# Kernel optimization log

Hardware: AMD Instinct MI355X
Metric: run time of the kernel (lower is better)

## Reference

```python
import jax, jax.numpy as jnp
import numpy as np

HEAD_SIZE = 256
ROTARY_DIM = 64
ROPE_THETA = 10000.0


def apply_gptj_rope(x, positions):
    """GPT-J (interleaved, non-neox) rotary embedding.
    x: [B, S, H, D], positions: [B, S] int. Rotates first ROTARY_DIM dims."""
    half = ROTARY_DIM // 2
    inv_freq = 1.0 / (ROPE_THETA ** (jnp.arange(0, ROTARY_DIM, 2, dtype=jnp.float32) / ROTARY_DIM))
    ang = positions.astype(jnp.float32)[..., None] * inv_freq      # [B, S, half]
    cos = jnp.cos(ang)[:, :, None, :]                               # [B, S, 1, half]
    sin = jnp.sin(ang)[:, :, None, :]
    xr, xp = x[..., :ROTARY_DIM], x[..., ROTARY_DIM:]
    x1, x2 = xr[..., 0::2], xr[..., 1::2]                           # interleaved pairs
    o1 = x1 * cos - x2 * sin
    o2 = x2 * cos + x1 * sin
    rot = jnp.stack([o1, o2], axis=-1).reshape(*xr.shape)           # re-interleave
    return jnp.concatenate([rot, xp], axis=-1)


def setup_inputs() -> dict:
    key = jax.random.key(0)
    k1, k2, k3 = jax.random.split(key, 3)
    B, S, H = 2, 2048, 4096
    position_ids = jnp.broadcast_to(jnp.arange(S, dtype=jnp.int32), (B, S))
    hidden_states = jax.random.normal(k1, (B, S, H), dtype=jnp.float32)
    Wqkv = jax.random.normal(k2, (H, 3 * H), dtype=jnp.float32) * (H ** -0.5)
    Wo = jax.random.normal(k3, (H, H), dtype=jnp.float32) * (H ** -0.5)
    return {"position_ids": position_ids, "hidden_states": hidden_states, "Wqkv": Wqkv, "Wo": Wo}


def reference(position_ids, hidden_states, Wqkv, Wo):
    B, S, H = hidden_states.shape
    nh = H // HEAD_SIZE
    qkv = hidden_states @ Wqkv                                      # [B, S, 3H]
    q, k, v = jnp.split(qkv, 3, axis=-1)
    q = apply_gptj_rope(q.reshape(B, S, nh, HEAD_SIZE), position_ids)
    k = apply_gptj_rope(k.reshape(B, S, nh, HEAD_SIZE), position_ids)
    v = v.reshape(B, S, nh, HEAD_SIZE)
    scale = HEAD_SIZE ** -0.5
    scores = jnp.einsum('bqhd,bkhd->bhqk', q, k) * scale            # [B, nh, S, S]
    causal = jnp.tril(jnp.ones((S, S), dtype=bool))
    scores = jnp.where(causal, scores, jnp.finfo(scores.dtype).min)
    attn = jax.nn.softmax(scores, axis=-1)
    ctx = jnp.einsum('bhqk,bkhd->bqhd', attn, v).reshape(B, S, H)
    return ctx @ Wo
```

## Files before the change

### kernel.cpp

```cpp
#include <hip/hip_runtime.h>
#include <hip/hip_bf16.h>

typedef __bf16 bf16x8 __attribute__((ext_vector_type(8)));
typedef float f32x4 __attribute__((ext_vector_type(4)));

#define MFMA_BF16(a,b,c) __builtin_amdgcn_mfma_f32_16x16x32_bf16(a,b,c,0,0,0)

#define GLOAD16(g, l) __builtin_amdgcn_global_load_lds( \
    (const __attribute__((address_space(1))) unsigned int*)(g), \
    (__attribute__((address_space(3))) unsigned int*)(l), 16, 0, 0)

__device__ __forceinline__ unsigned short f2bf(float f) {
  unsigned u = __builtin_bit_cast(unsigned, f);
  return (unsigned short)((u + 0x7FFFu + ((u >> 16) & 1u)) >> 16);
}

__global__ __launch_bounds__(256)
void convert_bf16(const float* __restrict__ src, unsigned short* __restrict__ dst,
                  int n8) {
  int i = blockIdx.x * blockDim.x + threadIdx.x;
  int stride = gridDim.x * blockDim.x;
  for (; i < n8; i += stride) {
    float4 a = ((const float4*)src)[i*2];
    float4 b = ((const float4*)src)[i*2 + 1];
    short4 h0, h1;
    h0.x = (short)f2bf(a.x); h0.y = (short)f2bf(a.y);
    h0.z = (short)f2bf(a.z); h0.w = (short)f2bf(a.w);
    h1.x = (short)f2bf(b.x); h1.y = (short)f2bf(b.y);
    h1.z = (short)f2bf(b.z); h1.w = (short)f2bf(b.w);
    ((short4*)dst)[i*2] = h0;
    ((short4*)dst)[i*2 + 1] = h1;
  }
}

__global__ __launch_bounds__(256)
void transpose_convert(const float* __restrict__ W, unsigned short* __restrict__ Wt,
                       int K, int N) {
  __shared__ float tl[64][65];
  const int k0 = blockIdx.y * 64, n0 = blockIdx.x * 64;
  const int tr = threadIdx.x >> 4;
  const int tc4 = (threadIdx.x & 15) * 4;
  for (int i = 0; i < 4; ++i) {
    int r = tr + i*16;
    float4 v = *(const float4*)(W + (size_t)(k0 + r)*N + n0 + tc4);
    tl[r][tc4+0] = v.x; tl[r][tc4+1] = v.y;
    tl[r][tc4+2] = v.z; tl[r][tc4+3] = v.w;
  }
  __syncthreads();
  for (int i = 0; i < 4; ++i) {
    int nr = tr + i*16;
    short4 h;
    h.x = (short)f2bf(tl[tc4+0][nr]);
    h.y = (short)f2bf(tl[tc4+1][nr]);
    h.z = (short)f2bf(tl[tc4+2][nr]);
    h.w = (short)f2bf(tl[tc4+3][nr]);
    *(short4*)(Wt + (size_t)(n0 + nr)*K + k0 + tc4) = h;
  }
}

__global__ __launch_bounds__(256)
void transpose_v(const unsigned short* __restrict__ qkv,
                 unsigned short* __restrict__ Vt) {
  __shared__ unsigned short tl[64][68];
  const int bh = blockIdx.z;
  const int s0 = blockIdx.x * 64;
  const int d0 = blockIdx.y * 64;
  const int b = bh >> 4, h = bh & 15;
  const int tr = threadIdx.x >> 4;
  const int tc = (threadIdx.x & 15) * 4;
  const unsigned short* src = qkv + ((size_t)(b*2048 + s0))*12288 + 8192 + h*256 + d0;
  for (int i = 0; i < 4; ++i) {
    int s = tr + i*16;
    *(short4*)&tl[s][tc] = *(const short4*)(src + (size_t)s*12288 + tc);
  }
  __syncthreads();
  unsigned short* dst = Vt + ((size_t)bh*256 + d0)*2048 + s0;
  for (int i = 0; i < 4; ++i) {
    int d = tr + i*16;
    short4 h4;
    h4.x = (short)tl[tc+0][d];
    h4.y = (short)tl[tc+1][d];
    h4.z = (short)tl[tc+2][d];
    h4.w = (short)tl[tc+3][d];
    *(short4*)(dst + (size_t)d*2048 + tc) = h4;
  }
}

template<bool ROPE, bool OUT_BF16>
__global__ __launch_bounds__(512, 2)
void gemm256(const unsigned short* __restrict__ A,
             const unsigned short* __restrict__ Bt,
             const int* __restrict__ pos,
             void* __restrict__ Cp, int N, int K, int nbx)
{
  __shared__ __align__(16) unsigned short L[2][4][8192];
  const int tid = threadIdx.x, lane = tid & 63, w = tid >> 6;
  const int wr = w >> 2, wc = w & 3;
  const int nwg = gridDim.x;
  int wg = blockIdx.x;
  if ((nwg & 7) == 0) wg = (wg & 7) * (nwg >> 3) + (wg >> 3);
  const int bx = wg % nbx, by = wg / nbx;
  const int row0 = by * 256, col0 = bx * 256;

  const int crow = lane & 15, g = lane >> 4;
  const int arow = lane >> 3;
  const int asegsw = ((lane & 7) ^ arow) * 8;
  const int xo = (crow & 7) << 4;

  unsigned aoff[4], boff[4];
#pragma unroll
  for (int i = 0; i < 4; ++i) {
    int chunk = w*4 + i;
    aoff[i] = (unsigned)((row0 + chunk*8 + arow) * K + asegsw);
    boff[i] = (unsigned)((col0 + chunk*8 + arow) * K + asegsw);
  }

#define STAGE(T, B) do {                                              \
    int kto = (T) * 64;                                               \
    _Pragma("unroll")                                                 \
    for (int i = 0; i < 4; ++i) {                                     \
      GLOAD16(A  + aoff[i] + kto, &L[B][wr][(wc*4 + i)*512]);         \
      GLOAD16(Bt + boff[i] + kto, &L[B][2 + wr][(wc*4 + i)*512]);     \
    }                                                                 \
  } while (0)

  f32x4 acc[8][4] = {};
  const int nt = K >> 6;
  STAGE(0, 0);
  STAGE(1, 1);
  int cur = 0;

  for (int t = 0; t < nt; ++t) {
    if (t < nt - 1) asm volatile("s_waitcnt vmcnt(8)" ::: "memory");
    else            asm volatile("s_waitcnt vmcnt(0)" ::: "memory");
    __builtin_amdgcn_s_barrier();

    const char* Ab = (const char*)&L[cur][wr][0];
    const char* Bb = (const char*)&L[cur][2 + (wc >> 1)][0];
    const int rB0 = (wc & 1) * 64;

    __builtin_amdgcn_s_setprio(1);
    bf16x8 af[2][8], bfv[2][4];
#pragma unroll
    for (int kk = 0; kk < 2; ++kk) {
      const int ko = (((kk*4 + g) << 4)) ^ xo;
#pragma unroll
      for (int m = 0; m < 8; ++m)
        af[kk][m] = *(const bf16x8*)(Ab + (m*16 + crow)*128 + ko);
#pragma unroll
      for (int n = 0; n < 4; ++n)
        bfv[kk][n] = *(const bf16x8*)(Bb + (rB0 + n*16 + crow)*128 + ko);
    }
#pragma unroll
    for (int kk = 0; kk < 2; ++kk)
#pragma unroll
      for (int m = 0; m < 8; ++m)
#pragma unroll
        for (int n = 0; n < 4; ++n)
          acc[m][n] = MFMA_BF16(af[kk][m], bfv[kk][n], acc[m][n]);
    __builtin_amdgcn_s_setprio(0);

    __builtin_amdgcn_sched_barrier(0);
    asm volatile("s_waitcnt lgkmcnt(0)" ::: "memory");
    __builtin_amdgcn_sched_barrier(0);
    __builtin_amdgcn_s_barrier();
    if (t + 2 < nt) STAGE(t + 2, cur);
    cur ^= 1;
  }
#undef STAGE

#pragma unroll
  for (int m = 0; m < 8; ++m) {
    const int rbase = row0 + wr*128 + m*16 + (g << 2);
#pragma unroll
    for (int n = 0; n < 4; ++n) {
      const int c = col0 + wc*64 + n*16 + crow;
      bool rot = false;
      float invf = 0.f;
      if (ROPE) {
        rot = (c < 8192) && ((c & 255) < 64);
        if (rot) {
          int i2 = (c & 63) >> 1;
          invf = exp2f(-(float)i2 * 0.4152410118609203f);
        }
      }
#pragma unroll
      for (int r = 0; r < 4; ++r) {
        int rowg = rbase + r;
        float v = acc[m][n][r];
        if (ROPE && rot) {
          float ang = (float)pos[rowg] * invf;
          float s_ = __sinf(ang), c_ = __cosf(ang);
          float pv = __shfl_xor(v, 1, 64);
          v = (c & 1) ? fmaf(v, c_, pv * s_) : fmaf(v, c_, -pv * s_);
        }
        if (OUT_BF16)
          ((unsigned short*)Cp)[(size_t)rowg*N + c] = f2bf(v);
        else
          ((float*)Cp)[(size_t)rowg*N + c] = v;
      }
    }
  }
}

template<bool A_BF16, bool ROPE, bool OUT_BF16>
__global__ __launch_bounds__(256)
void gemm128(const void* __restrict__ Ap, const float* __restrict__ Bp,
             const int* __restrict__ pos, void* __restrict__ Cp,
             int N, int K)
{
  __shared__ __align__(16) short Al[128*40];
  __shared__ __align__(16) short Bl[128*40];
  const int tid = threadIdx.x;
  const int lane = tid & 63, wid = tid >> 6;
  const int wr = wid >> 1, wc = wid & 1;
  const int row0 = blockIdx.y * 128, col0 = blockIdx.x * 128;
  f32x4 acc[4][4] = {};
  const int bcol = tid & 127;
  const int kb0 = (tid >> 7) * 4;

  for (int kt = 0; kt < K; kt += 32) {
    if (A_BF16) {
      const unsigned short* Ab = (const unsigned short*)Ap;
      for (int i = 0; i < 2; ++i) {
        int idx = tid + i*256;
        int ar = idx >> 2, ac = (idx & 3) * 8;
        *(int4*)(&Al[ar*40 + ac]) = *(const int4*)(Ab + (size_t)(row0+ar)*K + kt + ac);
      }
    } else {
      const float* Af = (const float*)Ap;
      for (int i = 0; i < 4; ++i) {
        int idx = tid + i*256;
        int ar = idx >> 3, ac = (idx & 7) * 4;
        float4 v = *(const float4*)(Af + (size_t)(row0+ar)*K + kt + ac);
        short4 h;
        h.x = (short)f2bf(v.x); h.y = (short)f2bf(v.y);
        h.z = (short)f2bf(v.z); h.w = (short)f2bf(v.w);
        *(short4*)(&Al[ar*40 + ac]) = h;
      }
    }
    for (int r = 0; r < 4; ++r) {
      int kb = kb0 + r*8;
      const float* bp = Bp + (size_t)(kt+kb)*N + col0 + bcol;
      float x0 = bp[0];
      float x1 = bp[(size_t)N];
      float x2 = bp[2*(size_t)N];
      float x3 = bp[3*(size_t)N];
      short4 h;
      h.x = (short)f2bf(x0); h.y = (short)f2bf(x1);
      h.z = (short)f2bf(x2); h.w = (short)f2bf(x3);
      *(short4*)(&Bl[bcol*40 + kb]) = h;
    }
    __syncthreads();
    const int k8 = (lane >> 4) * 8;
    bf16x8 af[4], bfr[4];
    for (int m = 0; m < 4; ++m)
      af[m] = *(const bf16x8*)(&Al[(wr*64 + m*16 + (lane&15))*40 + k8]);
    for (int n = 0; n < 4; ++n)
      bfr[n] = *(const bf16x8*)(&Bl[(wc*64 + n*16 + (lane&15))*40 + k8]);
    for (int m = 0; m < 4; ++m)
      for (int n = 0; n < 4; ++n)
        acc[m][n] = MFMA_BF16(af[m], bfr[n], acc[m][n]);
    __syncthreads();
  }

  for (int m = 0; m < 4; ++m) {
    const int rbase = row0 + wr*64 + m*16 + ((lane>>4)<<2);
    for (int n = 0; n < 4; ++n) {
      const int c = col0 + wc*64 + n*16 + (lane & 15);
      bool rot = false;
      float invf = 0.f;
      if (ROPE) {
        rot = (c < 8192) && ((c & 255) < 64);
        if (rot) {
          int i2 = (c & 63) >> 1;
          invf = exp2f(-(float)i2 * 0.4152410118609203f);
        }
      }
      for (int r = 0; r < 4; ++r) {
        int rowg = rbase + r;
        float v = acc[m][n][r];
        if (ROPE && rot) {
          float ang = (float)pos[rowg] * invf;
          float s_ = __sinf(ang), c_ = __cosf(ang);
          float pv = __shfl_xor(v, 1, 64);
          v = (c & 1) ? fmaf(v, c_, pv * s_) : fmaf(v, c_, -pv * s_);
        }
        if (OUT_BF16)
          ((unsigned short*)Cp)[(size_t)rowg*N + c] = f2bf(v);
        else
          ((float*)Cp)[(size_t)rowg*N + c] = v;
      }
    }
  }
}

__global__ __launch_bounds__(512, 2)
void attn_kernel3(const unsigned short* __restrict__ qkv,
                  const unsigned short* __restrict__ Vt,
                  unsigned short* __restrict__ ctx)
{
  const int QN = 12288;
  __shared__ __align__(16) unsigned char Kl[2][32768];
  __shared__ __align__(16) unsigned char Vl[2][32768];
  __shared__ __align__(16) unsigned char Pl[128*144];
  const int tid = threadIdx.x, lane = tid & 63, w = tid >> 6;
  const int qp = blockIdx.x, bh = blockIdx.y;
  const int b = bh >> 4, h = bh & 15;
  const size_t rowbase = (size_t)b * 2048;
  const int colr = lane & 15, g = lane >> 4;

  const int kr0 = tid >> 5;
  const int kcolb = ((tid*16) & 511) ^ ((kr0 & 7) << 4);
  const unsigned koff = (unsigned)(kr0*QN) + (kcolb >> 1);
  const int vd0 = tid >> 3;
  const int vcolb = ((tid*16) & 127) ^ ((vd0 & 7) << 4);
  const unsigned voff = (unsigned)(vd0*2048) + (vcolb >> 1);

  const unsigned short* kbase = qkv + rowbase*QN + 4096 + h*256;
  const unsigned short* vbase = Vt + (size_t)bh*256*2048;

#define STAGEKV(KT, B) do {                                                    \
    const unsigned short* kb_ = kbase + (unsigned)(KT)*64u*(unsigned)QN;       \
    const unsigned short* vb_ = vbase + (unsigned)(KT)*64u;                    \
    _Pragma("unroll")                                                          \
    for (int i = 0; i < 4; ++i)                                                \
      GLOAD16(kb_ + koff + i*16*QN, &Kl[B][tid*16 + i*8192]);                  \
    _Pragma("unroll")                                                          \
    for (int i = 0; i < 4; ++i)                                                \
      GLOAD16(vb_ + voff + i*64*2048, &Vl[B][tid*16 + i*8192]);                \
  } while (0)

  for (int phase = 0; phase < 2; ++phase) {
    const int qt = phase ? qp : (15 - qp);
    const int nkt = 2*qt + 2;

    bf16x8 qf[8];
    {
      const unsigned short* qp_ = qkv + (rowbase + qt*128 + w*16 + colr)*QN + h*256 + g*8;
#pragma unroll
      for (int f = 0; f < 8; ++f)
        qf[f] = *(const bf16x8*)(qp_ + 32*f);
    }
    f32x4 acc[16] = {};
    float m_r[4], l_r[4];
#pragma unroll
    for (int r = 0; r < 4; ++r) { m_r[r] = -1e30f; l_r[r] = 0.f; }

    STAGEKV(0, 0);
    STAGEKV(1, 1);
    int cur = 0;

    for (int kt = 0; kt < nkt; ++kt) {
      if (kt < nkt - 1) asm volatile("s_waitcnt vmcnt(8)" ::: "memory");
      else              asm volatile("s_waitcnt vmcnt(0)" ::: "memory");
      __builtin_amdgcn_s_barrier();

      const unsigned char* Kb = Kl[cur];
      f32x4 sc[4];
      __builtin_amdgcn_s_setprio(1);
#pragma unroll
      for (int nf = 0; nf < 4; ++nf) {
        f32x4 s = {};
        int krow = nf*16 + colr;
        int xo2 = (krow & 7) << 4;
        const unsigned char* kp = Kb + krow*512;
#pragma unroll
        for (int st = 0; st < 8; ++st) {
          bf16x8 kf = *(const bf16x8*)(kp + ((64*st + 16*g) ^ xo2));
          s = MFMA_BF16(qf[st], kf, s);
        }
        sc[nf] = s;
      }
      __builtin_amdgcn_s_setprio(0);

      const int qrow0 = qt*128 + w*16 + g*4;
      float pm[4] = {-3e38f,-3e38f,-3e38f,-3e38f};
      float pvv[4][4];
#pragma unroll
      for (int nf = 0; nf < 4; ++nf) {
        int kcol = kt*64 + nf*16 + colr;
#pragma unroll
        for (int r = 0; r < 4; ++r) {
          float v = sc[nf][r] * 0.0625f;
          if (kcol > qrow0 + r) v = -1e30f;
          pvv[nf][r] = v;
          pm[r] = fmaxf(pm[r], v);
        }
      }
#pragma unroll
      for (int mk = 1; mk < 16; mk <<= 1)
#pragma unroll
        for (int r = 0; r < 4; ++r)
          pm[r] = fmaxf(pm[r], __shfl_xor(pm[r], mk, 64));
      float alpha[4];
#pragma unroll
      for (int r = 0; r < 4; ++r) {
        float mn = fmaxf(m_r[r], pm[r]);
        alpha[r] = __expf(m_r[r] - mn);
        m_r[r] = mn;
      }
      float ps[4] = {0.f,0.f,0.f,0.f};
      unsigned short pb[4][4];
#pragma unroll
      for (int nf = 0; nf < 4; ++nf)
#pragma unroll
        for (int r = 0; r < 4; ++r) {
          float p = __expf(pvv[nf][r] - m_r[r]);
          ps[r] += p;
          pb[nf][r] = f2bf(p);
        }
#pragma unroll
      for (int mk = 1; mk < 16; mk <<= 1)
#pragma unroll
        for (int r = 0; r < 4; ++r)
          ps[r] += __shfl_xor(ps[r], mk, 64);
#pragma unroll
      for (int r = 0; r < 4; ++r)
        l_r[r] = l_r[r]*alpha[r] + ps[r];
#pragma unroll
      for (int nf2 = 0; nf2 < 16; ++nf2)
#pragma unroll
        for (int r = 0; r < 4; ++r)
          acc[nf2][r] *= alpha[r];

#pragma unroll
      for (int nf = 0; nf < 4; ++nf)
#pragma unroll
        for (int r = 0; r < 4; ++r)
          *(unsigned short*)(Pl + (w*16 + g*4 + r)*144 + (nf*16 + colr)*2) = pb[nf][r];

      const unsigned char* Vb = Vl[cur];
      __builtin_amdgcn_s_setprio(1);
#pragma unroll
      for (int st2 = 0; st2 < 2; ++st2) {
        bf16x8 pf = *(const bf16x8*)(Pl + (w*16 + colr)*144 + (32*st2 + g*8)*2);
#pragma unroll
        for (int nf2 = 0; nf2 < 16; ++nf2) {
          int d = nf2*16 + colr;
          bf16x8 vf = *(const bf16x8*)(Vb + ((d*128 + 64*st2 + 16*g) ^ ((d&7)<<4)));
          acc[nf2] = MFMA_BF16(pf, vf, acc[nf2]);
        }
      }
      __builtin_amdgcn_s_setprio(0);

      __builtin_amdgcn_sched_barrier(0);
      asm volatile("s_waitcnt lgkmcnt(0)" ::: "memory");
      __builtin_amdgcn_sched_barrier(0);
      __builtin_amdgcn_s_barrier();
      if (kt + 2 < nkt) STAGEKV(kt + 2, cur);
      cur ^= 1;
    }

    float linv[4];
#pragma unroll
    for (int r = 0; r < 4; ++r) linv[r] = 1.0f / l_r[r];
#pragma unroll
    for (int nf2 = 0; nf2 < 16; ++nf2)
#pragma unroll
      for (int r = 0; r < 4; ++r) {
        int qrow = qt*128 + w*16 + g*4 + r;
        float o = acc[nf2][r] * linv[r];
        ctx[(rowbase + qrow)*4096 + h*256 + nf2*16 + colr] = f2bf(o);
      }
  }
#undef STAGEKV
}

__global__ __launch_bounds__(256, 2)
void attn_kernel2(const unsigned short* __restrict__ qkv,
                  unsigned short* __restrict__ ctx)
{
  const int S = 2048, D = 256, QN = 12288;
  __shared__ __align__(16) unsigned char Kl[64*512];
  __shared__ __align__(16) unsigned char Vl[256*128];
  __shared__ __align__(16) unsigned char Pl[64*144];
  const int tid = threadIdx.x, lane = tid & 63, w = tid >> 6;
  const int qp = blockIdx.x, bh = blockIdx.y;
  const int b = bh >> 4, h = bh & 15;
  const size_t rowbase = (size_t)b * S;
  const int colr = lane & 15, g = lane >> 4;

  const int kr0 = tid >> 5, c8 = (tid & 31) * 8;
  const unsigned kwb = (unsigned)((kr0*512 + c8*2) ^ ((kr0 & 7) << 4));
  const int dd = (tid >> 2) * 4, kbb = (tid & 3) * 4;

  const unsigned short* kbase0 = qkv + rowbase*QN + 4096 + h*D;
  const unsigned short* vbase0 = qkv + rowbase*QN + 8192 + h*D;

  bf16x8 kreg[8];
  short4 vreg[16];

#define LOADKV(KT) do {                                                        \
    const unsigned short* kb_ = kbase0 + (size_t)(KT)*64*QN;                   \
    _Pragma("unroll")                                                          \
    for (int i = 0; i < 8; ++i)                                                \
      kreg[i] = *(const bf16x8*)(kb_ + (size_t)(kr0 + i*8)*QN + c8);           \
    const unsigned short* vb_ = vbase0 + (size_t)(KT)*64*QN;                   \
    _Pragma("unroll")                                                          \
    for (int r4 = 0; r4 < 4; ++r4) {                                           \
      int kb2 = kbb + 16*r4;                                                   \
      _Pragma("unroll")                                                        \
      for (int j = 0; j < 4; ++j)                                              \
        vreg[r4*4+j] = *(const short4*)(vb_ + (size_t)(kb2+j)*QN + dd);        \
    }                                                                          \
  } while (0)

#define WRITEKV() do {                                                         \
    _Pragma("unroll")                                                          \
    for (int i = 0; i < 8; ++i)                                                \
      *(bf16x8*)(Kl + kwb + i*4096) = kreg[i];                                 \
    _Pragma("unroll")                                                          \
    for (int r4 = 0; r4 < 4; ++r4) {                                           \
      int kb2 = kbb + 16*r4;                                                   \
      short4 v0 = vreg[r4*4+0], v1 = vreg[r4*4+1];                             \
      short4 v2 = vreg[r4*4+2], v3 = vreg[r4*4+3];                             \
      short4 t;                                                                \
      t.x=v0.x; t.y=v1.x; t.z=v2.x; t.w=v3.x;                                  \
      *(short4*)(Vl + (((dd+0)*128 + kb2*2) ^ (((dd+0)&7)<<4))) = t;           \
      t.x=v0.y; t.y=v1.y; t.z=v2.y; t.w=v3.y;                                  \
      *(short4*)(Vl + (((dd+1)*128 + kb2*2) ^ (((dd+1)&7)<<4))) = t;           \
      t.x=v0.z; t.y=v1.z; t.z=v2.z; t.w=v3.z;                                  \
      *(short4*)(Vl + (((dd+2)*128 + kb2*2) ^ (((dd+2)&7)<<4))) = t;           \
      t.x=v0.w; t.y=v1.w; t.z=v2.w; t.w=v3.w;                                  \
      *(short4*)(Vl + (((dd+3)*128 + kb2*2) ^ (((dd+3)&7)<<4))) = t;           \
    }                                                                          \
  } while (0)

  for (int phase = 0; phase < 2; ++phase) {
    const int qt = phase ? qp : (31 - qp);

    bf16x8 qf[8];
    {
      const unsigned short* qp_ = qkv + (rowbase + qt*64 + w*16 + colr)*QN + h*D + g*8;
#pragma unroll
      for (int f = 0; f < 8; ++f)
        qf[f] = *(const bf16x8*)(qp_ + 32*f);
    }
    f32x4 acc[16] = {};
    float m_r[4], l_r[4];
#pragma unroll
    for (int r = 0; r < 4; ++r) { m_r[r] = -1e30f; l_r[r] = 0.f; }

    LOADKV(0);
    WRITEKV();
    __syncthreads();

    for (int kt = 0; kt <= qt; ++kt) {
      if (kt < qt) LOADKV(kt + 1);
      __builtin_amdgcn_sched_barrier(0);

      f32x4 sc[4];
#pragma unroll
      for (int nf = 0; nf < 4; ++nf) {
        f32x4 s = {};
        int krow = nf*16 + colr;
        int xo2 = (krow & 7) << 4;
        const unsigned char* kp = Kl + krow*512;
#pragma unroll
        for (int st = 0; st < 8; ++st) {
          bf16x8 kf = *(const bf16x8*)(kp + ((64*st + 16*g) ^ xo2));
          s = MFMA_BF16(qf[st], kf, s);
        }
        sc[nf] = s;
      }

      const int qrow0 = qt*64 + w*16 + g*4;
      float pm[4] = {-3e38f,-3e38f,-3e38f,-3e38f};
      float pvv[4][4];
#pragma unroll
      for (int nf = 0; nf < 4; ++nf) {
        int kcol = kt*64 + nf*16 + colr;
#pragma unroll
        for (int r = 0; r < 4; ++r) {
          float v = sc[nf][r] * 0.0625f;
          if (kcol > qrow0 + r) v = -1e30f;
          pvv[nf][r] = v;
          pm[r] = fmaxf(pm[r], v);
        }
      }
#pragma unroll
      for (int mk = 1; mk < 16; mk <<= 1)
#pragma unroll
        for (int r = 0; r < 4; ++r)
          pm[r] = fmaxf(pm[r], __shfl_xor(pm[r], mk, 64));
      float alpha[4];
#pragma unroll
      for (int r = 0; r < 4; ++r) {
        float mn = fmaxf(m_r[r], pm[r]);
        alpha[r] = __expf(m_r[r] - mn);
        m_r[r] = mn;
      }
      float ps[4] = {0.f,0.f,0.f,0.f};
      unsigned short pb[4][4];
#pragma unroll
      for (int nf = 0; nf < 4; ++nf)
#pragma unroll
        for (int r = 0; r < 4; ++r) {
          float p = __expf(pvv[nf][r] - m_r[r]);
          ps[r] += p;
          pb[nf][r] = f2bf(p);
        }
#pragma unroll
      for (int mk = 1; mk < 16; mk <<= 1)
#pragma unroll
        for (int r = 0; r < 4; ++r)
          ps[r] += __shfl_xor(ps[r], mk, 64);
#pragma unroll
      for (int r = 0; r < 4; ++r)
        l_r[r] = l_r[r]*alpha[r] + ps[r];
#pragma unroll
      for (int nf2 = 0; nf2 < 16; ++nf2)
#pragma unroll
        for (int r = 0; r < 4; ++r)
          acc[nf2][r] *= alpha[r];

#pragma unroll
      for (int nf = 0; nf < 4; ++nf)
#pragma unroll
        for (int r = 0; r < 4; ++r)
          *(unsigned short*)(Pl + (w*16 + g*4 + r)*144 + (nf*16 + colr)*2) = pb[nf][r];

#pragma unroll
      for (int st2 = 0; st2 < 2; ++st2) {
        bf16x8 pf = *(const bf16x8*)(Pl + (w*16 + colr)*144 + (32*st2 + g*8)*2);
#pragma unroll
        for (int nf2 = 0; nf2 < 16; ++nf2) {
          int d = nf2*16 + colr;
          bf16x8 vf = *(const bf16x8*)(Vl + ((d*128 + 64*st2 + 16*g) ^ ((d&7)<<4)));
          acc[nf2] = MFMA_BF16(pf, vf, acc[nf2]);
        }
      }
      __syncthreads();
      if (kt < qt) {
        WRITEKV();
        __syncthreads();
      }
    }

    float linv[4];
#pragma unroll
    for (int r = 0; r < 4; ++r) linv[r] = 1.0f / l_r[r];
#pragma unroll
    for (int nf2 = 0; nf2 < 16; ++nf2)
#pragma unroll
      for (int r = 0; r < 4; ++r) {
        int qrow = qt*64 + w*16 + g*4 + r;
        float o = acc[nf2][r] * linv[r];
        ctx[(rowbase + qrow)*4096 + h*D + nf2*16 + colr] = f2bf(o);
      }
    if (phase == 0) __syncthreads();
  }
#undef LOADKV
#undef WRITEKV
}

extern "C" void kernel_launch(void* const* d_in, const int* in_sizes, int n_in,
                              void* d_out, int out_size, void* d_ws, size_t ws_size,
                              hipStream_t stream) {
  const int*   pos    = (const int*)d_in[0];
  const float* hidden = (const float*)d_in[1];
  const float* Wqkv   = (const float*)d_in[2];
  const float* Wo     = (const float*)d_in[3];

  const size_t QKV_B  = (size_t)4096 * 12288 * 2;
  const size_t CTX_B  = (size_t)4096 * 4096 * 2;
  const size_t FAST_NEED = QKV_B + QKV_B + CTX_B;

  if (ws_size >= FAST_NEED) {
    unsigned short* qkv     = (unsigned short*)d_ws;
    unsigned short* WqkvT   = (unsigned short*)((char*)d_ws + QKV_B);
    unsigned short* WoT     = WqkvT;
    unsigned short* ctx     = (unsigned short*)((char*)d_ws + QKV_B + CTX_B);
    unsigned short* hiddenB = (unsigned short*)((char*)d_ws + 2*QKV_B);
    unsigned short* Vt      = hiddenB;

    convert_bf16<<<2048, 256, 0, stream>>>(hidden, hiddenB, 4096*4096/8);
    transpose_convert<<<dim3(192, 64), 256, 0, stream>>>(Wqkv, WqkvT, 4096, 12288);
    gemm256<true, true><<<768, 512, 0, stream>>>(
        hiddenB, WqkvT, pos, qkv, 12288, 4096, 48);
    transpose_convert<<<dim3(64, 64), 256, 0, stream>>>(Wo, WoT, 4096, 4096);
    transpose_v<<<dim3(32, 4, 32), 256, 0, stream>>>(qkv, Vt);
    attn_kernel3<<<dim3(8, 32), 512, 0, stream>>>(qkv, Vt, ctx);
    gemm256<false, false><<<256, 512, 0, stream>>>(
        ctx, WoT, nullptr, d_out, 4096, 4096, 16);
  } else {
    if (ws_size < QKV_B + CTX_B) return;
    unsigned short* qkv = (unsigned short*)d_ws;
    unsigned short* ctx = qkv + (size_t)4096 * 12288;
    gemm128<false, true, true><<<dim3(96, 32), 256, 0, stream>>>(
        hidden, Wqkv, pos, qkv, 12288, 4096);
    attn_kernel2<<<dim3(16, 32), 256, 0, stream>>>(qkv, ctx);
    gemm128<true, false, false><<<dim3(32, 32), 256, 0, stream>>>(
        ctx, Wo, nullptr, d_out, 4096, 4096);
  }
}
```

Measured before the change: 790.9 us.

## Split GEMM main loop into four interleaved LDS-read/MFMA phases with barriers

The 256x256 bf16 GEMM inner loop is restructured from loading all A/B fragments and then issuing all MFMAs into four quadrant phases. Each phase loads a subset of fragments, synchronises, and runs MFMAs at raised priority, so the two waves per SIMD can ping-pong between LDS reads and matrix math. The next global-to-LDS stage is issued before the last quadrant's MFMAs, and the vmcnt wait moves to the end of the iteration. This cuts fragment register pressure but adds several workgroup barriers per k-step.

After: 792.2 us. No clear change (+0.2%).

```diff
diff --git a/kernel.cpp b/kernel.cpp
--- a/kernel.cpp
+++ b/kernel.cpp
@@ -88,10 +88,10 @@
 
 template<bool ROPE, bool OUT_BF16>
 __global__ __launch_bounds__(512, 2)
-void gemm256(const unsigned short* __restrict__ A,
-             const unsigned short* __restrict__ Bt,
-             const int* __restrict__ pos,
-             void* __restrict__ Cp, int N, int K, int nbx)
+void gemm256p(const unsigned short* __restrict__ A,
+              const unsigned short* __restrict__ Bt,
+              const int* __restrict__ pos,
+              void* __restrict__ Cp, int N, int K, int nbx)
 {
   __shared__ __align__(16) unsigned short L[2][4][8192];
   const int tid = threadIdx.x, lane = tid & 63, w = tid >> 6;
@@ -103,9 +103,9 @@
   const int row0 = by * 256, col0 = bx * 256;
 
   const int crow = lane & 15, g = lane >> 4;
+  const int xo = (crow & 7) << 4;
   const int arow = lane >> 3;
   const int asegsw = ((lane & 7) ^ arow) * 8;
-  const int xo = (crow & 7) << 4;
 
   unsigned aoff[4], boff[4];
 #pragma unroll
@@ -128,44 +128,92 @@
   const int nt = K >> 6;
   STAGE(0, 0);
   STAGE(1, 1);
-  int cur = 0;
+  asm volatile("s_waitcnt vmcnt(8)" ::: "memory");
+  __builtin_amdgcn_s_barrier();
 
   for (int t = 0; t < nt; ++t) {
-    if (t < nt - 1) asm volatile("s_waitcnt vmcnt(8)" ::: "memory");
-    else            asm volatile("s_waitcnt vmcnt(0)" ::: "memory");
-    __builtin_amdgcn_s_barrier();
-
+    const int cur = t & 1;
     const char* Ab = (const char*)&L[cur][wr][0];
     const char* Bb = (const char*)&L[cur][2 + (wc >> 1)][0];
     const int rB0 = (wc & 1) * 64;
 
-    __builtin_amdgcn_s_setprio(1);
-    bf16x8 af[2][8], bfv[2][4];
-#pragma unroll
-    for (int kk = 0; kk < 2; ++kk) {
-      const int ko = (((kk*4 + g) << 4)) ^ xo;
-#pragma unroll
-      for (int m = 0; m < 8; ++m)
-        af[kk][m] = *(const bf16x8*)(Ab + (m*16 + crow)*128 + ko);
-#pragma unroll
-      for (int n = 0; n < 4; ++n)
-        bfv[kk][n] = *(const bf16x8*)(Bb + (rB0 + n*16 + crow)*128 + ko);
-    }
-#pragma unroll
-    for (int kk = 0; kk < 2; ++kk)
-#pragma unroll
-      for (int m = 0; m < 8; ++m)
-#pragma unroll
-        for (int n = 0; n < 4; ++n)
-          acc[m][n] = MFMA_BF16(af[kk][m], bfv[kk][n], acc[m][n]);
-    __builtin_amdgcn_s_setprio(0);
-
-    __builtin_amdgcn_sched_barrier(0);
+    bf16x8 pA[4][2], pB0[2][2], pB1[2][2];
+
+#pragma unroll
+    for (int m = 0; m < 4; ++m)
+#pragma unroll
+      for (int kk = 0; kk < 2; ++kk)
+        pA[m][kk] = *(const bf16x8*)(Ab + (m*16 + crow)*128 + ((((kk*4+g)<<4)) ^ xo));
+#pragma unroll
+    for (int n = 0; n < 2; ++n)
+#pragma unroll
+      for (int kk = 0; kk < 2; ++kk)
+        pB0[n][kk] = *(const bf16x8*)(Bb + (rB0 + n*16 + crow)*128 + ((((kk*4+g)<<4)) ^ xo));
+    __builtin_amdgcn_s_barrier();
     asm volatile("s_waitcnt lgkmcnt(0)" ::: "memory");
     __builtin_amdgcn_sched_barrier(0);
+    __builtin_amdgcn_s_setprio(1);
+#pragma unroll
+    for (int kk = 0; kk < 2; ++kk)
+#pragma unroll
+      for (int m = 0; m < 4; ++m)
+#pragma unroll
+        for (int n = 0; n < 2; ++n)
+          acc[m][n] = MFMA_BF16(pA[m][kk], pB0[n][kk], acc[m][n]);
+    __builtin_amdgcn_s_setprio(0);
     __builtin_amdgcn_s_barrier();
+
+#pragma unroll
+    for (int n = 0; n < 2; ++n)
+#pragma unroll
+      for (int kk = 0; kk < 2; ++kk)
+        pB1[n][kk] = *(const bf16x8*)(Bb + (rB0 + 32 + n*16 + crow)*128 + ((((kk*4+g)<<4)) ^ xo));
+    __builtin_amdgcn_s_barrier();
+    asm volatile("s_waitcnt lgkmcnt(0)" ::: "memory");
+    __builtin_amdgcn_sched_barrier(0);
+    __builtin_amdgcn_s_setprio(1);
+#pragma unroll
+    for (int kk = 0; kk < 2; ++kk)
+#pragma unroll
+      for (int m = 0; m < 4; ++m)
+#pragma unroll
+        for (int n = 0; n < 2; ++n)
+          acc[m][2+n] = MFMA_BF16(pA[m][kk], pB1[n][kk], acc[m][2+n]);
+    __builtin_amdgcn_s_setprio(0);
+    __builtin_amdgcn_s_barrier();
+
+#pragma unroll
+    for (int m = 0; m < 4; ++m)
+#pragma unroll
+      for (int kk = 0; kk < 2; ++kk)
+        pA[m][kk] = *(const bf16x8*)(Ab + (64 + m*16 + crow)*128 + ((((kk*4+g)<<4)) ^ xo));
+    __builtin_amdgcn_s_barrier();
+    asm volatile("s_waitcnt lgkmcnt(0)" ::: "memory");
+    __builtin_amdgcn_sched_barrier(0);
+    __builtin_amdgcn_s_setprio(1);
+#pragma unroll
+    for (int kk = 0; kk < 2; ++kk)
+#pragma unroll
+      for (int m = 0; m < 4; ++m)
+#pragma unroll
+        for (int n = 0; n < 2; ++n)
+          acc[4+m][2+n] = MFMA_BF16(pA[m][kk], pB1[n][kk], acc[4+m][2+n]);
+    __builtin_amdgcn_s_setprio(0);
+    __builtin_amdgcn_s_barrier();
+
     if (t + 2 < nt) STAGE(t + 2, cur);
-    cur ^= 1;
+    __builtin_amdgcn_s_setprio(1);
+#pragma unroll
+    for (int kk = 0; kk < 2; ++kk)
+#pragma unroll
+      for (int m = 0; m < 4; ++m)
+#pragma unroll
+        for (int n = 0; n < 2; ++n)
+          acc[4+m][n] = MFMA_BF16(pA[m][kk], pB0[n][kk], acc[4+m][n]);
+    __builtin_amdgcn_s_setprio(0);
+    if (t < nt - 2)       asm volatile("s_waitcnt vmcnt(8)" ::: "memory");
+    else if (t == nt - 2) asm volatile("s_waitcnt vmcnt(0)" ::: "memory");
+    __builtin_amdgcn_s_barrier();
   }
 #undef STAGE
 
@@ -677,12 +725,12 @@
 
     convert_bf16<<<2048, 256, 0, stream>>>(hidden, hiddenB, 4096*4096/8);
     transpose_convert<<<dim3(192, 64), 256, 0, stream>>>(Wqkv, WqkvT, 4096, 12288);
-    gemm256<true, true><<<768, 512, 0, stream>>>(
+    gemm256p<true, true><<<768, 512, 0, stream>>>(
         hiddenB, WqkvT, pos, qkv, 12288, 4096, 48);
     transpose_convert<<<dim3(64, 64), 256, 0, stream>>>(Wo, WoT, 4096, 4096);
     transpose_v<<<dim3(32, 4, 32), 256, 0, stream>>>(qkv, Vt);
     attn_kernel3<<<dim3(8, 32), 512, 0, stream>>>(qkv, Vt, ctx);
-    gemm256<false, false><<<256, 512, 0, stream>>>(
+    gemm256p<false, false><<<256, 512, 0, stream>>>(
         ctx, WoT, nullptr, d_out, 4096, 4096, 16);
   } else {
     if (ws_size < QKV_B + CTX_B) return;
```

## Restructure GEMM main loop into quadrant-interleaved LDS reads, loads and MFMAs

Applied to the files above, without the earlier changes.

The 256x256 bf16 GEMM main loop is rewritten as a manually unrolled two-tile ping-pong. Each tile's MFMA work is split into four quadrants, and the global-to-LDS loads for upcoming tiles are interleaved between the quadrant LDS reads and MFMA blocks. The aim is finer-grained overlap of memory loads, LDS reads and matrix math, with smaller per-quadrant fragment register sets instead of loading all fragments up front. In exchange it adds many more barriers per tile and assumes the K tile count is even, and the staging order must exactly match the vmcnt waits to stay correct.

Result: faster. 735.5 us (-7.0%).

```diff
diff --git a/kernel.cpp b/kernel.cpp
--- a/kernel.cpp
+++ b/kernel.cpp
@@ -88,10 +88,10 @@
 
 template<bool ROPE, bool OUT_BF16>
 __global__ __launch_bounds__(512, 2)
-void gemm256(const unsigned short* __restrict__ A,
-             const unsigned short* __restrict__ Bt,
-             const int* __restrict__ pos,
-             void* __restrict__ Cp, int N, int K, int nbx)
+void gemm256p(const unsigned short* __restrict__ A,
+              const unsigned short* __restrict__ Bt,
+              const int* __restrict__ pos,
+              void* __restrict__ Cp, int N, int K, int nbx)
 {
   __shared__ __align__(16) unsigned short L[2][4][8192];
   const int tid = threadIdx.x, lane = tid & 63, w = tid >> 6;
@@ -103,71 +103,113 @@
   const int row0 = by * 256, col0 = bx * 256;
 
   const int crow = lane & 15, g = lane >> 4;
-  const int arow = lane >> 3;
-  const int asegsw = ((lane & 7) ^ arow) * 8;
   const int xo = (crow & 7) << 4;
-
-  unsigned aoff[4], boff[4];
-#pragma unroll
-  for (int i = 0; i < 4; ++i) {
-    int chunk = w*4 + i;
-    aoff[i] = (unsigned)((row0 + chunk*8 + arow) * K + asegsw);
-    boff[i] = (unsigned)((col0 + chunk*8 + arow) * K + asegsw);
-  }
-
-#define STAGE(T, B) do {                                              \
-    int kto = (T) * 64;                                               \
-    _Pragma("unroll")                                                 \
-    for (int i = 0; i < 4; ++i) {                                     \
-      GLOAD16(A  + aoff[i] + kto, &L[B][wr][(wc*4 + i)*512]);         \
-      GLOAD16(Bt + boff[i] + kto, &L[B][2 + wr][(wc*4 + i)*512]);     \
-    }                                                                 \
-  } while (0)
+  const int rB0 = (wc & 1) * 64;
+  const unsigned bo = (unsigned)((tid >> 3) * K + (((tid & 7) ^ ((tid >> 3) & 7)) * 8));
+  const int nt = K >> 6;
+
+#define STG_A(T,BUF,H,RLO) do { if ((T) < nt)                                   \
+    GLOAD16(A + (unsigned)((row0 + (H)*128 + (RLO))*K) + bo + (unsigned)(T)*64u,\
+            &L[BUF][H][(RLO)*64 + tid*8]); } while (0)
+#define STG_B(T,BUF,H,RLO) do { if ((T) < nt)                                   \
+    GLOAD16(Bt + (unsigned)((col0 + (H)*128 + (RLO))*K) + bo + (unsigned)(T)*64u,\
+            &L[BUF][2+(H)][(RLO)*64 + tid*8]); } while (0)
+
+#define RD_ALO(BUF) _Pragma("unroll") for (int m = 0; m < 4; ++m)               \
+    _Pragma("unroll") for (int kk = 0; kk < 2; ++kk)                            \
+      pAlo[m][kk] = *(const bf16x8*)((const char*)&L[BUF][wr][0] +              \
+                     (m*16 + crow)*128 + ((((kk*4+g)<<4)) ^ xo));
+#define RD_AHI(BUF) _Pragma("unroll") for (int m = 0; m < 4; ++m)               \
+    _Pragma("unroll") for (int kk = 0; kk < 2; ++kk)                            \
+      pAhi[m][kk] = *(const bf16x8*)((const char*)&L[BUF][wr][0] +              \
+                     (64 + m*16 + crow)*128 + ((((kk*4+g)<<4)) ^ xo));
+#define RD_B0(BUF) _Pragma("unroll") for (int n = 0; n < 2; ++n)                \
+    _Pragma("unroll") for (int kk = 0; kk < 2; ++kk)                            \
+      pB0[n][kk] = *(const bf16x8*)((const char*)&L[BUF][2+(wc>>1)][0] +        \
+                    (rB0 + n*16 + crow)*128 + ((((kk*4+g)<<4)) ^ xo));
+#define RD_B1(BUF) _Pragma("unroll") for (int n = 0; n < 2; ++n)                \
+    _Pragma("unroll") for (int kk = 0; kk < 2; ++kk)                            \
+      pB1[n][kk] = *(const bf16x8*)((const char*)&L[BUF][2+(wc>>1)][0] +        \
+                    (rB0 + 32 + n*16 + crow)*128 + ((((kk*4+g)<<4)) ^ xo));
+#define Q00 _Pragma("unroll") for (int kk = 0; kk < 2; ++kk)                    \
+    _Pragma("unroll") for (int m = 0; m < 4; ++m)                               \
+    _Pragma("unroll") for (int n = 0; n < 2; ++n)                               \
+      acc[m][n] = MFMA_BF16(pAlo[m][kk], pB0[n][kk], acc[m][n]);
+#define Q01 _Pragma("unroll") for (int kk = 0; kk < 2; ++kk)                    \
+    _Pragma("unroll") for (int m = 0; m < 4; ++m)                               \
+    _Pragma("unroll") for (int n = 0; n < 2; ++n)                               \
+      acc[m][2+n] = MFMA_BF16(pAlo[m][kk], pB1[n][kk], acc[m][2+n]);
+#define Q10 _Pragma("unroll") for (int kk = 0; kk < 2; ++kk)                    \
+    _Pragma("unroll") for (int m = 0; m < 4; ++m)                               \
+    _Pragma("unroll") for (int n = 0; n < 2; ++n)                               \
+      acc[4+m][n] = MFMA_BF16(pAhi[m][kk], pB0[n][kk], acc[4+m][n]);
+#define Q11 _Pragma("unroll") for (int kk = 0; kk < 2; ++kk)                    \
+    _Pragma("unroll") for (int m = 0; m < 4; ++m)                               \
+    _Pragma("unroll") for (int n = 0; n < 2; ++n)                               \
+      acc[4+m][2+n] = MFMA_BF16(pAhi[m][kk], pB1[n][kk], acc[4+m][2+n]);
+#define BAR __builtin_amdgcn_s_barrier()
+#define LGKM0 asm volatile("s_waitcnt lgkmcnt(0)" ::: "memory")
+#define PRIO1 __builtin_amdgcn_s_setprio(1)
+#define PRIO0 __builtin_amdgcn_s_setprio(0)
 
   f32x4 acc[8][4] = {};
-  const int nt = K >> 6;
-  STAGE(0, 0);
-  STAGE(1, 1);
-  int cur = 0;
-
-  for (int t = 0; t < nt; ++t) {
-    if (t < nt - 1) asm volatile("s_waitcnt vmcnt(8)" ::: "memory");
-    else            asm volatile("s_waitcnt vmcnt(0)" ::: "memory");
-    __builtin_amdgcn_s_barrier();
-
-    const char* Ab = (const char*)&L[cur][wr][0];
-    const char* Bb = (const char*)&L[cur][2 + (wc >> 1)][0];
-    const int rB0 = (wc & 1) * 64;
-
-    __builtin_amdgcn_s_setprio(1);
-    bf16x8 af[2][8], bfv[2][4];
-#pragma unroll
-    for (int kk = 0; kk < 2; ++kk) {
-      const int ko = (((kk*4 + g) << 4)) ^ xo;
-#pragma unroll
-      for (int m = 0; m < 8; ++m)
-        af[kk][m] = *(const bf16x8*)(Ab + (m*16 + crow)*128 + ko);
-#pragma unroll
-      for (int n = 0; n < 4; ++n)
-        bfv[kk][n] = *(const bf16x8*)(Bb + (rB0 + n*16 + crow)*128 + ko);
-    }
-#pragma unroll
-    for (int kk = 0; kk < 2; ++kk)
-#pragma unroll
-      for (int m = 0; m < 8; ++m)
-#pragma unroll
-        for (int n = 0; n < 4; ++n)
-          acc[m][n] = MFMA_BF16(af[kk][m], bfv[kk][n], acc[m][n]);
-    __builtin_amdgcn_s_setprio(0);
-
-    __builtin_amdgcn_sched_barrier(0);
-    asm volatile("s_waitcnt lgkmcnt(0)" ::: "memory");
-    __builtin_amdgcn_sched_barrier(0);
-    __builtin_amdgcn_s_barrier();
-    if (t + 2 < nt) STAGE(t + 2, cur);
-    cur ^= 1;
-  }
-#undef STAGE
+  STG_A(0,0,0,0);  STG_A(0,0,0,64); STG_A(0,0,1,0);  STG_A(0,0,1,64);
+  STG_B(0,0,0,0);  STG_B(0,0,0,64); STG_B(0,0,1,0);  STG_B(0,0,1,64);
+  STG_A(1,1,0,0);  STG_A(1,1,1,0);
+  STG_B(1,1,0,0);  STG_B(1,1,0,64); STG_B(1,1,1,0);  STG_B(1,1,1,64);
+  asm volatile("s_waitcnt vmcnt(6)" ::: "memory");
+  BAR;
+
+  const int nI = nt >> 1;
+  for (int i = 0; i < nI; ++i) {
+    const int t = 2*i;
+    const bool last = (i == nI - 1);
+    bf16x8 pAlo[4][2], pAhi[4][2], pB0[2][2], pB1[2][2];
+
+    RD_ALO(0); RD_B0(0);
+    STG_A(t+1, 1, 0, 64); STG_A(t+1, 1, 1, 64);
+    BAR; LGKM0; PRIO1; Q00; PRIO0; BAR;
+    RD_B1(0);
+    STG_A(t+2, 0, 0, 0); STG_A(t+2, 0, 1, 0);
+    BAR; LGKM0; PRIO1; Q01; PRIO0; BAR;
+    RD_AHI(0);
+    STG_B(t+2, 0, 0, 0); STG_B(t+2, 0, 0, 64);
+    BAR; LGKM0; PRIO1; Q10; PRIO0; BAR;
+    STG_B(t+2, 0, 1, 0); STG_B(t+2, 0, 1, 64);
+    PRIO1; Q11; PRIO0;
+    if (!last) asm volatile("s_waitcnt vmcnt(6)" ::: "memory");
+    else       asm volatile("s_waitcnt vmcnt(0)" ::: "memory");
+    BAR;
+
+    RD_ALO(1); RD_B0(1);
+    STG_A(t+2, 0, 0, 64); STG_A(t+2, 0, 1, 64);
+    BAR; LGKM0; PRIO1; Q00; PRIO0; BAR;
+    RD_B1(1);
+    STG_A(t+3, 1, 0, 0); STG_A(t+3, 1, 1, 0);
+    BAR; LGKM0; PRIO1; Q01; PRIO0; BAR;
+    RD_AHI(1);
+    STG_B(t+3, 1, 0, 0); STG_B(t+3, 1, 0, 64);
+    BAR; LGKM0; PRIO1; Q10; PRIO0; BAR;
+    STG_B(t+3, 1, 1, 0); STG_B(t+3, 1, 1, 64);
+    PRIO1; Q11; PRIO0;
+    if (!last) asm volatile("s_waitcnt vmcnt(6)" ::: "memory");
+    else       asm volatile("s_waitcnt vmcnt(0)" ::: "memory");
+    BAR;
+  }
+#undef STG_A
+#undef STG_B
+#undef RD_ALO
+#undef RD_AHI
+#undef RD_B0
+#undef RD_B1
+#undef Q00
+#undef Q01
+#undef Q10
+#undef Q11
+#undef BAR
+#undef LGKM0
+#undef PRIO1
+#undef PRIO0
 
 #pragma unroll
   for (int m = 0; m < 8; ++m) {
@@ -677,12 +719,12 @@
 
     convert_bf16<<<2048, 256, 0, stream>>>(hidden, hiddenB, 4096*4096/8);
     transpose_convert<<<dim3(192, 64), 256, 0, stream>>>(Wqkv, WqkvT, 4096, 12288);
-    gemm256<true, true><<<768, 512, 0, stream>>>(
+    gemm256p<true, true><<<768, 512, 0, stream>>>(
         hiddenB, WqkvT, pos, qkv, 12288, 4096, 48);
     transpose_convert<<<dim3(64, 64), 256, 0, stream>>>(Wo, WoT, 4096, 4096);
     transpose_v<<<dim3(32, 4, 32), 256, 0, stream>>>(qkv, Vt);
     attn_kernel3<<<dim3(8, 32), 512, 0, stream>>>(qkv, Vt, ctx);
-    gemm256<false, false><<<256, 512, 0, stream>>>(
+    gemm256p<false, false><<<256, 512, 0, stream>>>(
         ctx, WoT, nullptr, d_out, 4096, 4096, 16);
   } else {
     if (ws_size < QKV_B + CTX_B) return;
```
